# Performance work log

Hardware: AMD Instinct MI355X
Metric: run time of the kernel (lower is better)

Reference implementation:

```python
import jax, jax.numpy as jnp
import numpy as np

N_NODES = 50000
N_EDGES = 800000
FEA_DIM = 128
N_LAYER = 3
ACTOR_H = 512
N_GRAPHS = 64


def gcn_conv(x, src, dst, W, b, n_nodes):
    """PyG GCNConv: add self-loops, symmetric deg normalization, linear, scatter-add.
    out[i] = sum_{j->i} d_j^{-1/2} d_i^{-1/2} (x_j W) + d_i^{-1} (x_i W) + b
    where d_i = in_degree(i) + 1 (self-loop included)."""
    h = x @ W  # [N, F]
    deg = jax.ops.segment_sum(jnp.ones(src.shape[0], x.dtype), dst, num_segments=n_nodes) + 1.0
    dinv = jax.lax.rsqrt(deg)  # [N]
    coef = (dinv[src] * dinv[dst])[:, None]  # [E, 1]
    agg = jax.ops.segment_sum(h[src] * coef, dst, num_segments=n_nodes)  # gather-scale-scatter
    agg = agg + h * (dinv * dinv)[:, None]  # self-loop term
    return agg + b


def setup_inputs() -> dict:
    key = jax.random.key(0)
    ks = jax.random.split(key, 12)
    x = jax.random.normal(ks[0], (N_NODES, FEA_DIM), dtype=jnp.float32)
    edge_index = jax.random.randint(ks[1], (2, N_EDGES), 0, N_NODES, dtype=jnp.int32)
    batch = jnp.sort(jax.random.randint(ks[2], (N_NODES,), 0, N_GRAPHS, dtype=jnp.int32))
    s = 1.0 / np.sqrt(FEA_DIM)
    conv_W = jax.random.normal(ks[3], (N_LAYER, FEA_DIM, FEA_DIM), dtype=jnp.float32) * s
    conv_b = jnp.zeros((N_LAYER, FEA_DIM), dtype=jnp.float32)
    fea_w1 = jax.random.normal(ks[4], (FEA_DIM, ACTOR_H), dtype=jnp.float32) * s
    fea_b1 = jnp.zeros((ACTOR_H,), dtype=jnp.float32)
    fea_w2 = jax.random.normal(ks[5], (ACTOR_H, FEA_DIM), dtype=jnp.float32) * (1.0 / np.sqrt(ACTOR_H))
    fea_b2 = jnp.zeros((FEA_DIM,), dtype=jnp.float32)
    node_w = jax.random.normal(ks[6], (FEA_DIM, 1), dtype=jnp.float32) * s
    node_b = jnp.zeros((1,), dtype=jnp.float32)
    return {"x": x, "edge_index": edge_index, "batch": batch,
            "conv_W": conv_W, "conv_b": conv_b,
            "fea_w1": fea_w1, "fea_b1": fea_b1,
            "fea_w2": fea_w2, "fea_b2": fea_b2,
            "node_w": node_w, "node_b": node_b}


def reference(x, edge_index, batch, conv_W, conv_b, fea_w1, fea_b1, fea_w2, fea_b2, node_w, node_b):
    src, dst = edge_index[0], edge_index[1]
    n_nodes = x.shape[0]
    for l in range(N_LAYER):  # fixed small layer loop
        x = jax.nn.relu(gcn_conv(x, src, dst, conv_W[l], conv_b[l], n_nodes))
    node_prob = jnp.squeeze(x @ node_w + node_b, axis=-1)  # [N]
    # global mean pool over graphs
    sums = jax.ops.segment_sum(x, batch, num_segments=N_GRAPHS)  # [G, F]
    cnts = jax.ops.segment_sum(jnp.ones(n_nodes, x.dtype), batch, num_segments=N_GRAPHS)
    fea = sums / jnp.maximum(cnts, 1.0)[:, None]
    fea = jax.nn.relu(fea @ fea_w1 + fea_b1)
    fea_prob = fea @ fea_w2 + fea_b2  # [G, F]
    return (node_prob, fea_prob)
```

## Files before the change

kernel.cpp:

```cpp
#include <hip/hip_runtime.h>

#define N_NODES 50000
#define N_EDGES 800000
#define FEA 128
#define NL 3
#define AH 512
#define NG 64
#define NBLK 196

typedef short bf16x8 __attribute__((ext_vector_type(8)));
typedef float f32x4 __attribute__((ext_vector_type(4)));
typedef uint  u32x4 __attribute__((ext_vector_type(4)));

__device__ __forceinline__ ushort f2bf(float f) {
    uint u = __float_as_uint(f);
    uint r = u + 0x7FFFu + ((u >> 16) & 1u);
    return (ushort)(r >> 16);
}
__device__ __forceinline__ float bf2f(ushort u) {
    return __uint_as_float((uint)u << 16);
}

#define DA 3125
#define DB (DA + 6250)
#define DC (DB + 192)
#define DD (DC + 1)
__global__ __launch_bounds__(256) void k_deg_prep(const int* __restrict__ dst,
                                                  int* __restrict__ deg,
                                                  ushort* __restrict__ rank,
                                                  const float* __restrict__ x,
                                                  ushort* __restrict__ Xhi,
                                                  ushort* __restrict__ Xlo,
                                                  const float* __restrict__ convW,
                                                  ushort* __restrict__ WhiT,
                                                  ushort* __restrict__ WloT,
                                                  ushort* __restrict__ H) {
    int blk = blockIdx.x;
    if (blk < DA) {
        int i = blk * 256 + threadIdx.x;
        rank[i] = (ushort)atomicAdd(&deg[dst[i]], 1);
    } else if (blk < DB) {
        int i4 = (blk - DA) * 1024 + threadIdx.x * 4;
        float4 v = *(const float4*)(x + i4);
        ushort h0 = f2bf(v.x), h1 = f2bf(v.y), h2 = f2bf(v.z), h3 = f2bf(v.w);
        uint2 hv, lv;
        hv.x = (uint)h0 | ((uint)h1 << 16);
        hv.y = (uint)h2 | ((uint)h3 << 16);
        lv.x = (uint)f2bf(v.x - bf2f(h0)) | ((uint)f2bf(v.y - bf2f(h1)) << 16);
        lv.y = (uint)f2bf(v.z - bf2f(h2)) | ((uint)f2bf(v.w - bf2f(h3)) << 16);
        *(uint2*)(Xhi + i4) = hv;
        *(uint2*)(Xlo + i4) = lv;
    } else if (blk < DC) {
        int t = (blk - DB) * 256 + threadIdx.x;
        int l = t >> 14, r = t & 16383;
        int k = r >> 7, c = r & 127;
        float w = convW[t];
        ushort h = f2bf(w);
        WhiT[(size_t)l * 16384 + c * FEA + k] = h;
        WloT[(size_t)l * 16384 + c * FEA + k] = f2bf(w - bf2f(h));
    } else {
        if (threadIdx.x < 64) ((uint*)(H + (size_t)N_NODES * FEA))[threadIdx.x] = 0;
    }
}

__device__ __forceinline__ int block_scan_incl(int v, int* wsum) {
    int lane = threadIdx.x & 63, w = threadIdx.x >> 6;
    int s = v;
#pragma unroll
    for (int off = 1; off < 64; off <<= 1) {
        int t = __shfl_up(s, off);
        if (lane >= off) s += t;
    }
    if (lane == 63) wsum[w] = s;
    __syncthreads();
    int woff = 0;
    for (int k = 0; k < w; ++k) woff += wsum[k];
    return woff + s;
}

__global__ __launch_bounds__(256) void k_scan1(const int* __restrict__ deg,
                                               int* __restrict__ rowptr,
                                               int* __restrict__ bsum,
                                               float* __restrict__ dinv) {
    __shared__ int wsum[4];
    int i = blockIdx.x * 256 + threadIdx.x;
    int v = (i < N_NODES) ? deg[i] : 0;
    int pv = (v + 7) & ~7;
    int incl = block_scan_incl(pv, wsum);
    if (i < N_NODES) {
        rowptr[i] = incl - pv;
        dinv[i] = rsqrtf((float)v + 1.0f);
    }
    if (threadIdx.x == 255) bsum[blockIdx.x] = incl;
}

__global__ __launch_bounds__(256) void k_scan2(int* __restrict__ bsum,
                                               int* __restrict__ boff,
                                               int* __restrict__ rowptr) {
    __shared__ int wsum[4];
    int v = (threadIdx.x < NBLK) ? bsum[threadIdx.x] : 0;
    int incl = block_scan_incl(v, wsum);
    if (threadIdx.x < NBLK) boff[threadIdx.x] = incl - v;
    if (threadIdx.x == NBLK - 1) rowptr[N_NODES] = incl;
}

__global__ __launch_bounds__(256) void k_scan3(int* __restrict__ rowptr,
                                               const int* __restrict__ boff) {
    int i = blockIdx.x * 256 + threadIdx.x;
    if (i < N_NODES) rowptr[i] += boff[blockIdx.x];
}

#define FA 3125
#define FB (FA + NBLK)
#define FC (FB + NBLK)
__global__ __launch_bounds__(256) void k_fill2(const int* __restrict__ src,
                                               const int* __restrict__ dst,
                                               const int* __restrict__ rowptr,
                                               const ushort* __restrict__ rank,
                                               const int* __restrict__ deg,
                                               const int* __restrict__ batch,
                                               ushort* __restrict__ eidx,
                                               int* __restrict__ gstart) {
    int blk = blockIdx.x;
    if (blk < FA) {
        int e = blk * 256 + threadIdx.x;
        eidx[rowptr[dst[e]] + (int)rank[e]] = (ushort)src[e];
    } else if (blk < FB) {
        int i = (blk - FA) * 256 + threadIdx.x;
        if (i < N_NODES) {
            int d = deg[i], r = rowptr[i];
            int pd = (d + 7) & ~7;
            for (int k = d; k < pd; ++k) eidx[r + k] = (ushort)N_NODES;
        }
    } else {
        int i = (blk - FB) * 256 + threadIdx.x;
        if (i < N_NODES) {
            int b = batch[i];
            int bp = (i == 0) ? -1 : batch[i - 1];
            for (int g = bp + 1; g <= b; ++g) gstart[g] = i;
            if (i == N_NODES - 1)
                for (int g = b + 1; g <= NG; ++g) gstart[g] = N_NODES;
        }
    }
}

__global__ __launch_bounds__(256) void k_gemm(const ushort* __restrict__ Xhi,
                                              const ushort* __restrict__ Xlo,
                                              const ushort* __restrict__ WhiT,
                                              const ushort* __restrict__ WloT,
                                              const float* __restrict__ dinv,
                                              ushort* __restrict__ H) {
    const int wv = threadIdx.x >> 6;
    const int lane = threadIdx.x & 63;
    const int lr = lane & 15;
    const int lk = lane >> 4;

    bf16x8 bhi[2][4], blo[2][4];
#pragma unroll
    for (int ct = 0; ct < 2; ++ct) {
        int col = wv * 32 + ct * 16 + lr;
#pragma unroll
        for (int kf = 0; kf < 4; ++kf) {
            bhi[ct][kf] = *(const bf16x8*)(WhiT + (size_t)col * FEA + kf * 32 + lk * 8);
            blo[ct][kf] = *(const bf16x8*)(WloT + (size_t)col * FEA + kf * 32 + lk * 8);
        }
    }

    for (int rt = blockIdx.x; rt < N_NODES / 16; rt += gridDim.x) {
        int r0 = rt * 16;
        const ushort* xh = Xhi + (size_t)(r0 + lr) * FEA;
        const ushort* xl = Xlo + (size_t)(r0 + lr) * FEA;
        bf16x8 ahi[4], alo[4];
#pragma unroll
        for (int kf = 0; kf < 4; ++kf) {
            ahi[kf] = *(const bf16x8*)(xh + kf * 32 + lk * 8);
            alo[kf] = *(const bf16x8*)(xl + kf * 32 + lk * 8);
        }
        f32x4 acc0 = {0.f, 0.f, 0.f, 0.f};
        f32x4 acc1 = {0.f, 0.f, 0.f, 0.f};
#pragma unroll
        for (int kf = 0; kf < 4; ++kf) {
            acc0 = __builtin_amdgcn_mfma_f32_16x16x32_bf16(ahi[kf], bhi[0][kf], acc0, 0, 0, 0);
            acc0 = __builtin_amdgcn_mfma_f32_16x16x32_bf16(ahi[kf], blo[0][kf], acc0, 0, 0, 0);
            acc0 = __builtin_amdgcn_mfma_f32_16x16x32_bf16(alo[kf], bhi[0][kf], acc0, 0, 0, 0);
            acc1 = __builtin_amdgcn_mfma_f32_16x16x32_bf16(ahi[kf], bhi[1][kf], acc1, 0, 0, 0);
            acc1 = __builtin_amdgcn_mfma_f32_16x16x32_bf16(ahi[kf], blo[1][kf], acc1, 0, 0, 0);
            acc1 = __builtin_amdgcn_mfma_f32_16x16x32_bf16(alo[kf], bhi[1][kf], acc1, 0, 0, 0);
        }
#pragma unroll
        for (int reg = 0; reg < 4; ++reg) {
            int orow = r0 + lk * 4 + reg;
            float s = dinv[orow];
            H[(size_t)orow * FEA + wv * 32 + lr]      = f2bf(acc0[reg] * s);
            H[(size_t)orow * FEA + wv * 32 + 16 + lr] = f2bf(acc1[reg] * s);
        }
    }
}

__global__ __launch_bounds__(256) void k_gather(const int* __restrict__ rowptr,
                                                const ushort* __restrict__ eidx,
                                                const float* __restrict__ dinv,
                                                const ushort* __restrict__ H,
                                                const float* __restrict__ b,
                                                ushort* __restrict__ Xhi,
                                                ushort* __restrict__ Xlo,
                                                const float* __restrict__ nw,
                                                const float* __restrict__ nbp,
                                                float* __restrict__ out_node,
                                                int last) {
    int t = blockIdx.x * 256 + threadIdx.x;
    int node = t >> 4;
    int c8 = t & 15;
    if (node >= N_NODES) return;
    const uint4* H4 = (const uint4*)H;
    int r0 = rowptr[node], r1 = rowptr[node + 1];

    float a[8] = {0.f, 0.f, 0.f, 0.f, 0.f, 0.f, 0.f, 0.f};
#define ACC8(u)                                                              \
    do {                                                                     \
        a[0] += __uint_as_float((u).x << 16);                                \
        a[1] += __uint_as_float((u).x & 0xffff0000u);                        \
        a[2] += __uint_as_float((u).y << 16);                                \
        a[3] += __uint_as_float((u).y & 0xffff0000u);                        \
        a[4] += __uint_as_float((u).z << 16);                                \
        a[5] += __uint_as_float((u).z & 0xffff0000u);                        \
        a[6] += __uint_as_float((u).w << 16);                                \
        a[7] += __uint_as_float((u).w & 0xffff0000u);                        \
    } while (0)

    uint4 sv = H4[(size_t)node * 16 + c8];
    ACC8(sv);

    for (int j = r0; j < r1; j += 8) {
        uint4 ev = *(const uint4*)(eidx + j);
        int s0 = ev.x & 0xffff, s1 = ev.x >> 16;
        int s2 = ev.y & 0xffff, s3 = ev.y >> 16;
        int s4 = ev.z & 0xffff, s5 = ev.z >> 16;
        int s6 = ev.w & 0xffff, s7 = ev.w >> 16;
        uint4 h0 = H4[(size_t)s0 * 16 + c8];
        uint4 h1 = H4[(size_t)s1 * 16 + c8];
        uint4 h2 = H4[(size_t)s2 * 16 + c8];
        uint4 h3 = H4[(size_t)s3 * 16 + c8];
        uint4 h4 = H4[(size_t)s4 * 16 + c8];
        uint4 h5 = H4[(size_t)s5 * 16 + c8];
        uint4 h6 = H4[(size_t)s6 * 16 + c8];
        uint4 h7 = H4[(size_t)s7 * 16 + c8];
        ACC8(h0); ACC8(h1); ACC8(h2); ACC8(h3);
        ACC8(h4); ACC8(h5); ACC8(h6); ACC8(h7);
    }
#undef ACC8

    float di = dinv[node];
    const float4* b4 = (const float4*)b;
    float4 bb0 = b4[c8 * 2], bb1 = b4[c8 * 2 + 1];
    float o[8];
    o[0] = fmaxf(a[0] * di + bb0.x, 0.f);
    o[1] = fmaxf(a[1] * di + bb0.y, 0.f);
    o[2] = fmaxf(a[2] * di + bb0.z, 0.f);
    o[3] = fmaxf(a[3] * di + bb0.w, 0.f);
    o[4] = fmaxf(a[4] * di + bb1.x, 0.f);
    o[5] = fmaxf(a[5] * di + bb1.y, 0.f);
    o[6] = fmaxf(a[6] * di + bb1.z, 0.f);
    o[7] = fmaxf(a[7] * di + bb1.w, 0.f);

    if (last) {
        const float4* nw4 = (const float4*)nw;
        float4 n0 = nw4[c8 * 2], n1 = nw4[c8 * 2 + 1];
        float dot = o[0] * n0.x + o[1] * n0.y + o[2] * n0.z + o[3] * n0.w
                  + o[4] * n1.x + o[5] * n1.y + o[6] * n1.z + o[7] * n1.w;
        dot += __shfl_xor(dot, 1);
        dot += __shfl_xor(dot, 2);
        dot += __shfl_xor(dot, 4);
        dot += __shfl_xor(dot, 8);
        if (c8 == 0) out_node[node] = dot + nbp[0];
    }

    ushort hs[8];
    uint ls[8];
#pragma unroll
    for (int i = 0; i < 8; ++i) {
        hs[i] = f2bf(o[i]);
        ls[i] = f2bf(o[i] - bf2f(hs[i]));
    }
    u32x4 hv, lv;
    hv.x = (uint)hs[0] | ((uint)hs[1] << 16);
    hv.y = (uint)hs[2] | ((uint)hs[3] << 16);
    hv.z = (uint)hs[4] | ((uint)hs[5] << 16);
    hv.w = (uint)hs[6] | ((uint)hs[7] << 16);
    lv.x = ls[0] | (ls[1] << 16);
    lv.y = ls[2] | (ls[3] << 16);
    lv.z = ls[4] | (ls[5] << 16);
    lv.w = ls[6] | (ls[7] << 16);
    __builtin_nontemporal_store(hv, (u32x4*)(Xhi + (size_t)node * FEA + c8 * 8));
    __builtin_nontemporal_store(lv, (u32x4*)(Xlo + (size_t)node * FEA + c8 * 8));
}

__global__ __launch_bounds__(256) void k_pool(const ushort* __restrict__ Xhi,
                                              const ushort* __restrict__ Xlo,
                                              const int* __restrict__ gstart,
                                              float* __restrict__ psum_part) {
    int g = blockIdx.x >> 4, p = blockIdx.x & 15;
    int s = gstart[g], e = gstart[g + 1];
    int len = e - s;
    int lp = (len + 15) >> 4;
    int ps = s + p * lp, pe = min(ps + lp, e);
    int q = threadIdx.x >> 6, lane = threadIdx.x & 63;
    float2 acc = {0.f, 0.f};
    for (int node = ps + q; node < pe; node += 4) {
        uint hv = *(const uint*)(Xhi + (size_t)node * FEA + lane * 2);
        uint lv = *(const uint*)(Xlo + (size_t)node * FEA + lane * 2);
        acc.x += bf2f((ushort)hv) + bf2f((ushort)lv);
        acc.y += bf2f((ushort)(hv >> 16)) + bf2f((ushort)(lv >> 16));
    }
    __shared__ float lds[4 * FEA];
    lds[q * FEA + lane * 2 + 0] = acc.x;
    lds[q * FEA + lane * 2 + 1] = acc.y;
    __syncthreads();
    if (threadIdx.x < FEA) {
        psum_part[(size_t)blockIdx.x * FEA + threadIdx.x] =
            lds[threadIdx.x] + lds[FEA + threadIdx.x] +
            lds[2 * FEA + threadIdx.x] + lds[3 * FEA + threadIdx.x];
    }
}

__global__ __launch_bounds__(256) void k_mlp1(const float* __restrict__ psum_part,
                                              const int* __restrict__ gstart,
                                              const float* __restrict__ w1,
                                              const float* __restrict__ b1,
                                              float* __restrict__ h1ws) {
    __shared__ float feas[NG * 132];
    for (int idx = threadIdx.x; idx < NG * FEA; idx += 256) {
        int g = idx >> 7, f = idx & 127;
        const float* pp = psum_part + (size_t)g * 16 * FEA + f;
        float sum = 0.f;
#pragma unroll
        for (int p = 0; p < 16; ++p) sum += pp[p * FEA];
        float cnt = fmaxf((float)(gstart[g + 1] - gstart[g]), 1.0f);
        feas[g * 132 + f] = sum / cnt;
    }
    __syncthreads();
    int g = threadIdx.x >> 2, jj = threadIdx.x & 3;
    int j = blockIdx.x * 4 + jj;
    const float* fr = feas + g * 132;
    float a0 = 0.f, a1 = 0.f, a2 = 0.f, a3 = 0.f;
#pragma unroll 8
    for (int k = 0; k < FEA; k += 4) {
        a0 += fr[k + 0] * w1[(k + 0) * AH + j];
        a1 += fr[k + 1] * w1[(k + 1) * AH + j];
        a2 += fr[k + 2] * w1[(k + 2) * AH + j];
        a3 += fr[k + 3] * w1[(k + 3) * AH + j];
    }
    h1ws[(size_t)g * AH + j] = fmaxf((a0 + a1) + (a2 + a3) + b1[j], 0.f);
}

__global__ __launch_bounds__(256) void k_mlp2(const float* __restrict__ h1ws,
                                              const float* __restrict__ w2,
                                              const float* __restrict__ b2,
                                              float* __restrict__ out_fea) {
    int f = blockIdx.x;
    int g = threadIdx.x >> 2, q = threadIdx.x & 3;
    const float* hr = h1ws + (size_t)g * AH + q * 128;
    const float* wr = w2 + (size_t)q * 128 * FEA + f;
    float a0 = 0.f, a1 = 0.f, a2 = 0.f, a3 = 0.f;
#pragma unroll 8
    for (int k = 0; k < 128; k += 4) {
        a0 += hr[k + 0] * wr[(k + 0) * FEA];
        a1 += hr[k + 1] * wr[(k + 1) * FEA];
        a2 += hr[k + 2] * wr[(k + 2) * FEA];
        a3 += hr[k + 3] * wr[(k + 3) * FEA];
    }
    float p = (a0 + a1) + (a2 + a3);
    p += __shfl_xor(p, 1);
    p += __shfl_xor(p, 2);
    if (q == 0) out_fea[(size_t)g * FEA + f] = p + b2[f];
}

extern "C" void kernel_launch(void* const* d_in, const int* in_sizes, int n_in,
                              void* d_out, int out_size, void* d_ws, size_t ws_size,
                              hipStream_t stream) {
    const float* x     = (const float*)d_in[0];
    const int*   ei    = (const int*)d_in[1];
    const int*   batch = (const int*)d_in[2];
    const float* convW = (const float*)d_in[3];
    const float* convb = (const float*)d_in[4];
    const float* w1    = (const float*)d_in[5];
    const float* b1    = (const float*)d_in[6];
    const float* w2    = (const float*)d_in[7];
    const float* b2    = (const float*)d_in[8];
    const float* nw    = (const float*)d_in[9];
    const float* nb    = (const float*)d_in[10];
    float* out = (float*)d_out;

    char* wsb = (char*)d_ws;
    int*    deg    = (int*)wsb;
    float*  dinv   = (float*)(wsb + 50048ll * 4);
    int*    rowptr = (int*)(wsb + 100096ll * 4);
    int*    bsum   = (int*)(wsb + 150144ll * 4);
    int*    boff   = (int*)(wsb + 150344ll * 4);
    int*    gstart = (int*)(wsb + 150544ll * 4);
    int*    rankw  = (int*)(wsb + 150656ll * 4);
    ushort* rank   = (ushort*)rankw;
    float*  h1ws   = (float*)rankw;
    ushort* eidx   = (ushort*)(wsb + 950656ll * 4);
    ushort* H      = (ushort*)(wsb + 1600672ll * 4);
    ushort* Xhi    = (ushort*)(wsb + 4800736ll * 4);
    ushort* Xlo    = (ushort*)(wsb + 8000736ll * 4);
    float*  psum_part = (float*)(wsb + 11200736ll * 4);
    ushort* WhiT   = (ushort*)psum_part;
    ushort* WloT   = WhiT + 49152;

    const int* srcp = ei;
    const int* dstp = ei + N_EDGES;

    hipMemsetAsync(deg, 0, N_NODES * sizeof(int), stream);
    k_deg_prep<<<DD, 256, 0, stream>>>(dstp, deg, rank, x, Xhi, Xlo, convW, WhiT, WloT, H);
    k_scan1<<<NBLK, 256, 0, stream>>>(deg, rowptr, bsum, dinv);
    k_scan2<<<1, 256, 0, stream>>>(bsum, boff, rowptr);
    k_scan3<<<NBLK, 256, 0, stream>>>(rowptr, boff);
    k_fill2<<<FC, 256, 0, stream>>>(srcp, dstp, rowptr, rank, deg, batch, eidx, gstart);

    for (int l = 0; l < NL; ++l) {
        k_gemm<<<1024, 256, 0, stream>>>(Xhi, Xlo, WhiT + (size_t)l * 16384,
                                         WloT + (size_t)l * 16384, dinv, H);
        k_gather<<<(N_NODES * 16 + 255) / 256, 256, 0, stream>>>(
            rowptr, eidx, dinv, H, convb + (size_t)l * FEA, Xhi, Xlo,
            nw, nb, out, l == NL - 1 ? 1 : 0);
    }

    k_pool<<<NG * 16, 256, 0, stream>>>(Xhi, Xlo, gstart, psum_part);
    k_mlp1<<<128, 256, 0, stream>>>(psum_part, gstart, w1, b1, h1ws);
    k_mlp2<<<128, 256, 0, stream>>>(h1ws, w2, b2, out + N_NODES);
}
```

Before: 257.0 us.

## Slice node features into 16-byte channel planes to localize gather traffic

Stores H, Xhi and Xlo as 16 channel slices, each holding 8 features per node contiguously. Each gather block then serves a single slice, so its random neighbor reads land in a 0.8MB working set that fits in cache instead of the full feature table. The GEMM, prep and pool kernels are rewritten to address the sliced layout. The last-layer node-probability dot product moves out of the gather kernel into the pool kernel, using a wave reduction per node. The trade-off is less coalesced 16-byte GEMM and pool accesses and a shuffle reduction per node inside the pool loop.

New measurement: 333.7 us. +29.8%, slower.

```diff
diff --git a/kernel.cpp b/kernel.cpp
--- a/kernel.cpp
+++ b/kernel.cpp
@@ -21,8 +21,11 @@
     return __uint_as_float((uint)u << 16);
 }
 
+#define HSLICE ((size_t)(N_NODES + 1) * 8)
+#define XSLICE ((size_t)N_NODES * 8)
+
 #define DA 3125
-#define DB (DA + 6250)
+#define DB (DA + 3125)
 #define DC (DB + 192)
 #define DD (DC + 1)
 __global__ __launch_bounds__(256) void k_deg_prep(const int* __restrict__ dst,
@@ -40,16 +43,29 @@
         int i = blk * 256 + threadIdx.x;
         rank[i] = (ushort)atomicAdd(&deg[dst[i]], 1);
     } else if (blk < DB) {
-        int i4 = (blk - DA) * 1024 + threadIdx.x * 4;
-        float4 v = *(const float4*)(x + i4);
-        ushort h0 = f2bf(v.x), h1 = f2bf(v.y), h2 = f2bf(v.z), h3 = f2bf(v.w);
-        uint2 hv, lv;
-        hv.x = (uint)h0 | ((uint)h1 << 16);
-        hv.y = (uint)h2 | ((uint)h3 << 16);
-        lv.x = (uint)f2bf(v.x - bf2f(h0)) | ((uint)f2bf(v.y - bf2f(h1)) << 16);
-        lv.y = (uint)f2bf(v.z - bf2f(h2)) | ((uint)f2bf(v.w - bf2f(h3)) << 16);
-        *(uint2*)(Xhi + i4) = hv;
-        *(uint2*)(Xlo + i4) = lv;
+        int i = (blk - DA) * 256 + threadIdx.x;
+        int node = i >> 4, c = i & 15;
+        const float* xr = x + (size_t)node * FEA + c * 8;
+        float4 u0 = *(const float4*)xr;
+        float4 u1 = *(const float4*)(xr + 4);
+        float xs[8] = {u0.x, u0.y, u0.z, u0.w, u1.x, u1.y, u1.z, u1.w};
+        ushort hs[8]; uint ls[8];
+#pragma unroll
+        for (int k = 0; k < 8; ++k) {
+            hs[k] = f2bf(xs[k]);
+            ls[k] = f2bf(xs[k] - bf2f(hs[k]));
+        }
+        u32x4 hv, lv;
+        hv.x = (uint)hs[0] | ((uint)hs[1] << 16);
+        hv.y = (uint)hs[2] | ((uint)hs[3] << 16);
+        hv.z = (uint)hs[4] | ((uint)hs[5] << 16);
+        hv.w = (uint)hs[6] | ((uint)hs[7] << 16);
+        lv.x = ls[0] | (ls[1] << 16);
+        lv.y = ls[2] | (ls[3] << 16);
+        lv.z = ls[4] | (ls[5] << 16);
+        lv.w = ls[6] | (ls[7] << 16);
+        *(u32x4*)(Xhi + (size_t)c * XSLICE + (size_t)node * 8) = hv;
+        *(u32x4*)(Xlo + (size_t)c * XSLICE + (size_t)node * 8) = lv;
     } else if (blk < DC) {
         int t = (blk - DB) * 256 + threadIdx.x;
         int l = t >> 14, r = t & 16383;
@@ -59,7 +75,10 @@
         WhiT[(size_t)l * 16384 + c * FEA + k] = h;
         WloT[(size_t)l * 16384 + c * FEA + k] = f2bf(w - bf2f(h));
     } else {
-        if (threadIdx.x < 64) ((uint*)(H + (size_t)N_NODES * FEA))[threadIdx.x] = 0;
+        if (threadIdx.x < 64) {
+            int c = threadIdx.x >> 2, j = threadIdx.x & 3;
+            ((uint*)H)[(size_t)c * (HSLICE / 2) + (size_t)N_NODES * 4 + j] = 0;
+        }
     }
 }
 
@@ -166,15 +185,18 @@
         }
     }
 
+    const int c0 = (wv * 32 + lr) >> 3;
+    const int off = (wv * 32 + lr) & 7;
+    const int c1 = c0 + 2;
+
     for (int rt = blockIdx.x; rt < N_NODES / 16; rt += gridDim.x) {
         int r0 = rt * 16;
-        const ushort* xh = Xhi + (size_t)(r0 + lr) * FEA;
-        const ushort* xl = Xlo + (size_t)(r0 + lr) * FEA;
         bf16x8 ahi[4], alo[4];
 #pragma unroll
         for (int kf = 0; kf < 4; ++kf) {
-            ahi[kf] = *(const bf16x8*)(xh + kf * 32 + lk * 8);
-            alo[kf] = *(const bf16x8*)(xl + kf * 32 + lk * 8);
+            size_t ao = (size_t)(kf * 4 + lk) * XSLICE + (size_t)(r0 + lr) * 8;
+            ahi[kf] = *(const bf16x8*)(Xhi + ao);
+            alo[kf] = *(const bf16x8*)(Xlo + ao);
         }
         f32x4 acc0 = {0.f, 0.f, 0.f, 0.f};
         f32x4 acc1 = {0.f, 0.f, 0.f, 0.f};
@@ -191,8 +213,8 @@
         for (int reg = 0; reg < 4; ++reg) {
             int orow = r0 + lk * 4 + reg;
             float s = dinv[orow];
-            H[(size_t)orow * FEA + wv * 32 + lr]      = f2bf(acc0[reg] * s);
-            H[(size_t)orow * FEA + wv * 32 + 16 + lr] = f2bf(acc1[reg] * s);
+            H[(size_t)c0 * HSLICE + (size_t)orow * 8 + off] = f2bf(acc0[reg] * s);
+            H[(size_t)c1 * HSLICE + (size_t)orow * 8 + off] = f2bf(acc1[reg] * s);
         }
     }
 }
@@ -203,16 +225,11 @@
                                                 const ushort* __restrict__ H,
                                                 const float* __restrict__ b,
                                                 ushort* __restrict__ Xhi,
-                                                ushort* __restrict__ Xlo,
-                                                const float* __restrict__ nw,
-                                                const float* __restrict__ nbp,
-                                                float* __restrict__ out_node,
-                                                int last) {
-    int t = blockIdx.x * 256 + threadIdx.x;
-    int node = t >> 4;
-    int c8 = t & 15;
+                                                ushort* __restrict__ Xlo) {
+    int c = blockIdx.x & 15;
+    int node = (blockIdx.x >> 4) * 256 + threadIdx.x;
     if (node >= N_NODES) return;
-    const uint4* H4 = (const uint4*)H;
+    const uint4* Hs = (const uint4*)H + (size_t)c * (N_NODES + 1);
     int r0 = rowptr[node], r1 = rowptr[node + 1];
 
     float a[8] = {0.f, 0.f, 0.f, 0.f, 0.f, 0.f, 0.f, 0.f};
@@ -228,7 +245,7 @@
         a[7] += __uint_as_float((u).w & 0xffff0000u);                        \
     } while (0)
 
-    uint4 sv = H4[(size_t)node * 16 + c8];
+    uint4 sv = Hs[node];
     ACC8(sv);
 
     for (int j = r0; j < r1; j += 8) {
@@ -237,14 +254,14 @@
         int s2 = ev.y & 0xffff, s3 = ev.y >> 16;
         int s4 = ev.z & 0xffff, s5 = ev.z >> 16;
         int s6 = ev.w & 0xffff, s7 = ev.w >> 16;
-        uint4 h0 = H4[(size_t)s0 * 16 + c8];
-        uint4 h1 = H4[(size_t)s1 * 16 + c8];
-        uint4 h2 = H4[(size_t)s2 * 16 + c8];
-        uint4 h3 = H4[(size_t)s3 * 16 + c8];
-        uint4 h4 = H4[(size_t)s4 * 16 + c8];
-        uint4 h5 = H4[(size_t)s5 * 16 + c8];
-        uint4 h6 = H4[(size_t)s6 * 16 + c8];
-        uint4 h7 = H4[(size_t)s7 * 16 + c8];
+        uint4 h0 = Hs[s0];
+        uint4 h1 = Hs[s1];
+        uint4 h2 = Hs[s2];
+        uint4 h3 = Hs[s3];
+        uint4 h4 = Hs[s4];
+        uint4 h5 = Hs[s5];
+        uint4 h6 = Hs[s6];
+        uint4 h7 = Hs[s7];
         ACC8(h0); ACC8(h1); ACC8(h2); ACC8(h3);
         ACC8(h4); ACC8(h5); ACC8(h6); ACC8(h7);
     }
@@ -252,7 +269,7 @@
 
     float di = dinv[node];
     const float4* b4 = (const float4*)b;
-    float4 bb0 = b4[c8 * 2], bb1 = b4[c8 * 2 + 1];
+    float4 bb0 = b4[c * 2], bb1 = b4[c * 2 + 1];
     float o[8];
     o[0] = fmaxf(a[0] * di + bb0.x, 0.f);
     o[1] = fmaxf(a[1] * di + bb0.y, 0.f);
@@ -263,18 +280,6 @@
     o[6] = fmaxf(a[6] * di + bb1.z, 0.f);
     o[7] = fmaxf(a[7] * di + bb1.w, 0.f);
 
-    if (last) {
-        const float4* nw4 = (const float4*)nw;
-        float4 n0 = nw4[c8 * 2], n1 = nw4[c8 * 2 + 1];
-        float dot = o[0] * n0.x + o[1] * n0.y + o[2] * n0.z + o[3] * n0.w
-                  + o[4] * n1.x + o[5] * n1.y + o[6] * n1.z + o[7] * n1.w;
-        dot += __shfl_xor(dot, 1);
-        dot += __shfl_xor(dot, 2);
-        dot += __shfl_xor(dot, 4);
-        dot += __shfl_xor(dot, 8);
-        if (c8 == 0) out_node[node] = dot + nbp[0];
-    }
-
     ushort hs[8];
     uint ls[8];
 #pragma unroll
@@ -291,13 +296,16 @@
     lv.y = ls[2] | (ls[3] << 16);
     lv.z = ls[4] | (ls[5] << 16);
     lv.w = ls[6] | (ls[7] << 16);
-    __builtin_nontemporal_store(hv, (u32x4*)(Xhi + (size_t)node * FEA + c8 * 8));
-    __builtin_nontemporal_store(lv, (u32x4*)(Xlo + (size_t)node * FEA + c8 * 8));
+    __builtin_nontemporal_store(hv, (u32x4*)(Xhi + (size_t)c * XSLICE + (size_t)node * 8));
+    __builtin_nontemporal_store(lv, (u32x4*)(Xlo + (size_t)c * XSLICE + (size_t)node * 8));
 }
 
 __global__ __launch_bounds__(256) void k_pool(const ushort* __restrict__ Xhi,
                                               const ushort* __restrict__ Xlo,
                                               const int* __restrict__ gstart,
+                                              const float* __restrict__ nw,
+                                              const float* __restrict__ nbp,
+                                              float* __restrict__ out_node,
                                               float* __restrict__ psum_part) {
     int g = blockIdx.x >> 4, p = blockIdx.x & 15;
     int s = gstart[g], e = gstart[g + 1];
@@ -305,12 +313,22 @@
     int lp = (len + 15) >> 4;
     int ps = s + p * lp, pe = min(ps + lp, e);
     int q = threadIdx.x >> 6, lane = threadIdx.x & 63;
+    const ushort* hb = Xhi + (size_t)(lane >> 2) * XSLICE + (lane & 3) * 2;
+    const ushort* lb = Xlo + (size_t)(lane >> 2) * XSLICE + (lane & 3) * 2;
+    float2 w = ((const float2*)nw)[lane];
+    float nbv = nbp[0];
     float2 acc = {0.f, 0.f};
     for (int node = ps + q; node < pe; node += 4) {
-        uint hv = *(const uint*)(Xhi + (size_t)node * FEA + lane * 2);
-        uint lv = *(const uint*)(Xlo + (size_t)node * FEA + lane * 2);
-        acc.x += bf2f((ushort)hv) + bf2f((ushort)lv);
-        acc.y += bf2f((ushort)(hv >> 16)) + bf2f((ushort)(lv >> 16));
+        uint hv = *(const uint*)(hb + (size_t)node * 8);
+        uint lv = *(const uint*)(lb + (size_t)node * 8);
+        float2 v;
+        v.x = bf2f((ushort)hv) + bf2f((ushort)lv);
+        v.y = bf2f((ushort)(hv >> 16)) + bf2f((ushort)(lv >> 16));
+        acc.x += v.x; acc.y += v.y;
+        float dot = v.x * w.x + v.y * w.y;
+#pragma unroll
+        for (int off = 32; off; off >>= 1) dot += __shfl_down(dot, off);
+        if (lane == 0) out_node[node] = dot + nbv;
     }
     __shared__ float lds[4 * FEA];
     lds[q * FEA + lane * 2 + 0] = acc.x;
@@ -422,12 +440,11 @@
     for (int l = 0; l < NL; ++l) {
         k_gemm<<<1024, 256, 0, stream>>>(Xhi, Xlo, WhiT + (size_t)l * 16384,
                                          WloT + (size_t)l * 16384, dinv, H);
-        k_gather<<<(N_NODES * 16 + 255) / 256, 256, 0, stream>>>(
-            rowptr, eidx, dinv, H, convb + (size_t)l * FEA, Xhi, Xlo,
-            nw, nb, out, l == NL - 1 ? 1 : 0);
-    }
-
-    k_pool<<<NG * 16, 256, 0, stream>>>(Xhi, Xlo, gstart, psum_part);
+        k_gather<<<NBLK * 16, 256, 0, stream>>>(
+            rowptr, eidx, dinv, H, convb + (size_t)l * FEA, Xhi, Xlo);
+    }
+
+    k_pool<<<NG * 16, 256, 0, stream>>>(Xhi, Xlo, gstart, nw, nb, out, psum_part);
     k_mlp1<<<128, 256, 0, stream>>>(psum_part, gstart, w1, b1, h1ws);
     k_mlp2<<<128, 256, 0, stream>>>(h1ws, w2, b2, out + N_NODES);
 }
```
